# Optimization experiments

Hardware: AMD Instinct MI355X
Metric: run time of the kernel (lower is better)

Reference implementation:

```python
import jax, jax.numpy as jnp
import numpy as np

WIN = 9  # local window size per spatial dim

def _boxfilter3d(x):
    k = jnp.ones((1, 1, WIN, WIN, WIN), x.dtype) / float(WIN ** 3)
    return jax.lax.conv_general_dilated(
        x, k, window_strides=(1, 1, 1), padding='SAME',
        dimension_numbers=('NCDHW', 'OIDHW', 'NCDHW'))

def setup_inputs() -> dict:
    key = jax.random.key(0)
    k1, k2 = jax.random.split(key)
    shape = (2, 1, 160, 192, 160)
    y_true = jax.random.uniform(k1, shape, dtype=jnp.float32)
    y_pred = jax.random.uniform(k2, shape, dtype=jnp.float32)
    return {"y_true": y_true, "y_pred": y_pred}

def reference(y_true, y_pred):
    Ii, Ji = y_true, y_pred
    mu1 = _boxfilter3d(Ii)
    mu2 = _boxfilter3d(Ji)
    sigma1_sq = _boxfilter3d(Ii * Ii) - mu1 * mu1
    sigma2_sq = _boxfilter3d(Ji * Ji) - mu2 * mu2
    sigma12 = _boxfilter3d(Ii * Ji) - mu1 * mu2
    cc = (sigma12 * sigma12) / (sigma1_sq * sigma2_sq + 1e-5)
    return -jnp.mean(cc)
```

## Files before the change

### kernel.cpp

```cpp
#include <hip/hip_runtime.h>

#define DD 160
#define HH 192
#define WW 160
#define HWs (HH * WW)
#define NTOT 9830400.0f
#define DOUT 20
#define NIT  28
#define NBLK 960

#define SDRS 62
#define SDP  1492
#define HSRS 10
#define HSC  162
#define HSP  810

typedef float    v4 __attribute__((ext_vector_type(4)));
typedef _Float16 h4 __attribute__((ext_vector_type(4)));
typedef _Float16 h2 __attribute__((ext_vector_type(2)));
typedef _Float16 h8 __attribute__((ext_vector_type(8)));

__device__ __forceinline__ void block_sync_lds() {
    __builtin_amdgcn_s_waitcnt(0xc07f);
    __builtin_amdgcn_s_barrier();
}
__device__ __forceinline__ v4 up(h4 x) { return __builtin_convertvector(x, v4); }
__device__ __forceinline__ h4 dnp(v4 x) {
    h2 a = __builtin_bit_cast(h2, __builtin_amdgcn_cvt_pkrtz(x[0], x[1]));
    h2 b = __builtin_bit_cast(h2, __builtin_amdgcn_cvt_pkrtz(x[2], x[3]));
    return __builtin_shufflevector(a, b, 0, 1, 2, 3);
}

__global__ __launch_bounds__(256, 4) void kf(const float* __restrict__ I,
                                             const float* __restrict__ J,
                                             float* __restrict__ partial) {
    __shared__ __align__(16) h4 SDL[2 * SDP];
    __shared__ __align__(16) h4 HSL[2 * HSP];
    __shared__ float red[256];

    const int tid = threadIdx.x;
    const int bx = blockIdx.x, by = blockIdx.y, b = blockIdx.z;
    const int w0 = (bx % 5) * 32, h0 = (bx / 5) * 16;
    const int d0 = by * DOUT;
    const int bid = bx + 60 * (by + 8 * b);

    const int rt = tid ^ ((bx & 1) << 7);

    const bool p1 = rt < 240;
    const int r = rt / 10, g = rt % 10;
    const int gh = h0 - 4 + r, gw = w0 - 4 + g * 4;
    const bool colOK = p1 && gh >= 0 && gh < HH && gw >= 0 && gw < WW;
    const size_t colOff = (size_t)gh * WW + gw;
    const float* Ib = I + (size_t)b * DD * HWs + colOff;
    const float* Jb = J + (size_t)b * DD * HWs + colOff;
    const int sdwOff = r * SDRS + (r >> 3) * 2 + 6 * g;

    const bool p2 = rt < 100;
    const int g2 = rt % 10, ch2 = (rt / 10) % 5, hh0 = (rt / 50) * 8;
    const int sdrOff = hh0 * SDRS + (hh0 >> 3) * 2 + 6 * g2 +
                       (ch2 == 4 ? 4 + (g2 & 1) : ch2);
    const int hswOff = ch2 * HSC + hh0 * HSRS + g2;

    const bool p3 = rt >= 128;
    const int q3 = rt & 127;
    const int hh = q3 >> 3, sg = q3 & 7;
    const int hsrOff = hh * HSRS + sg;

    v4 sd0 = 0.f, sd1 = 0.f, sd2 = 0.f, sd3 = 0.f, sd4 = 0.f;
    h4 fI[10], fJ[10];
#pragma unroll
    for (int uu = 0; uu < 10; ++uu) { fI[uu] = (h4)(_Float16)0; fJ[uu] = (h4)(_Float16)0; }
    v4 pAI = 0.f, pAJ = 0.f, pBI = 0.f, pBJ = 0.f;
    float acc = 0.f;
    const float inv = 1.0f / 729.0f;

    {
        const int s0 = d0 - 4;
        if (colOK && s0 >= 0) {
            pAI = *(const v4*)(Ib + (size_t)s0 * HWs);
            pAJ = *(const v4*)(Jb + (size_t)s0 * HWs);
        }
        const int s1 = d0 - 3;
        if (colOK && s1 >= 0) {
            pBI = *(const v4*)(Ib + (size_t)s1 * HWs);
            pBJ = *(const v4*)(Jb + (size_t)s1 * HWs);
        }
    }

    for (int tb = 0; tb < 30; tb += 10) {
#pragma unroll
        for (int u = 0; u < 10; ++u) {
            const int t = tb + u;

            if (t < NIT && p1) {
                v4 curI, curJ;
                if ((u & 1) == 0) { curI = pAI; curJ = pAJ; }
                else              { curI = pBI; curJ = pBJ; }
                h4 cI = dnp(curI), cJ = dnp(curJ);
                v4 aI = up(cI), aJ = up(cJ);
                v4 dI = aI, dJv = aJ;
                v4 dII = aI * aI, dJJ = aJ * aJ, dIJ = aI * aJ;
                if (t >= 9) {
                    h4 oI = fI[(u + 1) % 10], oJ = fJ[(u + 1) % 10];
                    v4 bI = up(oI), bJ = up(oJ);
                    dI -= bI; dJv -= bJ;
                    dII -= bI * bI; dJJ -= bJ * bJ; dIJ -= bI * bJ;
                }
                fI[u] = cI; fJ[u] = cJ;
                sd0 += dI; sd1 += dJv; sd2 += dII; sd3 += dJJ; sd4 += dIJ;
                h4* const qb = &SDL[(t & 1) * SDP + sdwOff];
                h4 c0 = dnp(sd0), c1 = dnp(sd1), c2 = dnp(sd2), c3 = dnp(sd3);
                *(h8*)qb       = __builtin_shufflevector(c0, c1, 0,1,2,3,4,5,6,7);
                *(h8*)(qb + 2) = __builtin_shufflevector(c2, c3, 0,1,2,3,4,5,6,7);
                qb[4 + (g & 1)] = dnp(sd4);
                v4 nI = 0.f, nJ = 0.f;
                const int sn = d0 - 2 + t;
                if (t + 2 < NIT && colOK && sn >= 0 && sn < DD) {
                    nI = *(const v4*)(Ib + (size_t)sn * HWs);
                    nJ = *(const v4*)(Jb + (size_t)sn * HWs);
                }
                if ((u & 1) == 0) { pAI = nI; pAJ = nJ; }
                else              { pBI = nI; pBJ = nJ; }
            }

            if (t >= 1 && t <= NIT && p2) {
                const int par = (t - 1) & 1;
                const h4* const sdr = &SDL[par * SDP + sdrOff];
                h4* const hsw = &HSL[par * HSP + hswOff];
                h4 keep[7];
                h4 s = sdr[0];
                keep[0] = s;
#pragma unroll
                for (int k = 1; k < 9; ++k) {
                    h4 v = sdr[k * SDRS + (k >= 8 ? 2 : 0)];
                    if (k < 7) keep[k] = v;
                    s += v;
                }
                hsw[0] = s;
#pragma unroll
                for (int j = 1; j < 8; ++j) {
                    s += sdr[(j + 8) * SDRS + 2] - keep[j - 1];
                    hsw[j * HSRS] = s;
                }
            }

            if (t >= 10 && p3) {
                const h4* const hsr = &HSL[(t & 1) * HSP + hsrOff];
                float w[5][4];
#pragma unroll
                for (int c = 0; c < 5; ++c) {
                    v4 fa = up(hsr[c * HSC]);
                    v4 fb = up(hsr[c * HSC + 1]);
                    v4 fc = up(hsr[c * HSC + 2]);
                    float s = fa[0] + fa[1] + fa[2] + fa[3] +
                              fb[0] + fb[1] + fb[2] + fb[3] + fc[0];
                    w[c][0] = s;
                    s += fc[1] - fa[0]; w[c][1] = s;
                    s += fc[2] - fa[1]; w[c][2] = s;
                    s += fc[3] - fa[2]; w[c][3] = s;
                }
#pragma unroll
                for (int e = 0; e < 4; ++e) {
                    float mu1 = w[0][e] * inv, mu2 = w[1][e] * inv;
                    float g1  = fmaf(-mu1, mu1, w[2][e] * inv);
                    float g2v = fmaf(-mu2, mu2, w[3][e] * inv);
                    float g12 = fmaf(-mu1, mu2, w[4][e] * inv);
                    acc += __fdividef(g12 * g12, fmaf(g1, g2v, 1e-5f));
                }
            }

            block_sync_lds();
        }
    }

    red[tid] = acc;
    __syncthreads();
    if (tid < 128) red[tid] += red[tid + 128];
    __syncthreads();
    if (tid < 64) {
        float a = red[tid] + red[tid + 64];
#pragma unroll
        for (int off = 32; off > 0; off >>= 1) a += __shfl_down(a, off);
        if (tid == 0) partial[bid] = a;
    }
}

__global__ void k3_final(const float* __restrict__ partial,
                         float* __restrict__ out) {
    __shared__ float r[1024];
    const int i = threadIdx.x;
    r[i] = (i < NBLK) ? partial[i] : 0.f;
    __syncthreads();
    for (int off = 512; off > 0; off >>= 1) {
        if (i < off) r[i] += r[i + off];
        __syncthreads();
    }
    if (i == 0) out[0] = -r[0] * (1.0f / NTOT);
}

extern "C" void kernel_launch(void* const* d_in, const int* in_sizes, int n_in,
                              void* d_out, int out_size, void* d_ws, size_t ws_size,
                              hipStream_t stream) {
    (void)in_sizes; (void)n_in; (void)out_size; (void)ws_size;
    const float* I = (const float*)d_in[0];
    const float* J = (const float*)d_in[1];
    float* out     = (float*)d_out;
    float* partial = (float*)d_ws;

    dim3 grid(60, 8, 2);
    kf<<<grid, 256, 0, stream>>>(I, J, partial);
    k3_final<<<1, 1024, 0, stream>>>(partial, out);
}
```

Baseline: 163.0 us.

## Halve depth chunk per block, doubling grid, with single-slice prefetch and LDS re-reads

Reduces the output depth per block from 20 to 10 slices, so the grid doubles to 1920 blocks and each block iterates 18 steps instead of 28. The aim is more parallelism and better CU fill. The price is a larger share of halo work: each block now reads 18 input slices to produce 10 outputs, versus 28 for 20. The prefetch pipeline drops from two slices in flight to one, and the ring buffer shrinks to 9 entries. The H-sum stage now re-reads outgoing values from LDS instead of keeping them in registers, and the final reduction is extended to handle 1920 partials.

```diff
diff --git a/kernel.cpp b/kernel.cpp
--- a/kernel.cpp
+++ b/kernel.cpp
@@ -5,9 +5,9 @@
 #define WW 160
 #define HWs (HH * WW)
 #define NTOT 9830400.0f
-#define DOUT 20
-#define NIT  28
-#define NBLK 960
+#define DOUT 10
+#define NIT  18
+#define NBLK 1920
 
 #define SDRS 62
 #define SDP  1492
@@ -42,7 +42,7 @@
     const int bx = blockIdx.x, by = blockIdx.y, b = blockIdx.z;
     const int w0 = (bx % 5) * 32, h0 = (bx / 5) * 16;
     const int d0 = by * DOUT;
-    const int bid = bx + 60 * (by + 8 * b);
+    const int bid = bx + 60 * (by + 16 * b);
 
     const int rt = tid ^ ((bx & 1) << 7);
 
@@ -67,109 +67,95 @@
     const int hsrOff = hh * HSRS + sg;
 
     v4 sd0 = 0.f, sd1 = 0.f, sd2 = 0.f, sd3 = 0.f, sd4 = 0.f;
-    h4 fI[10], fJ[10];
-#pragma unroll
-    for (int uu = 0; uu < 10; ++uu) { fI[uu] = (h4)(_Float16)0; fJ[uu] = (h4)(_Float16)0; }
-    v4 pAI = 0.f, pAJ = 0.f, pBI = 0.f, pBJ = 0.f;
+    h4 fI[9], fJ[9];
+#pragma unroll
+    for (int uu = 0; uu < 9; ++uu) { fI[uu] = (h4)(_Float16)0; fJ[uu] = (h4)(_Float16)0; }
+    v4 pLI = 0.f, pLJ = 0.f;
     float acc = 0.f;
     const float inv = 1.0f / 729.0f;
 
     {
-        const int s0 = d0 - 4;
-        if (colOK && s0 >= 0) {
-            pAI = *(const v4*)(Ib + (size_t)s0 * HWs);
-            pAJ = *(const v4*)(Jb + (size_t)s0 * HWs);
+        const int si = d0 - 4;
+        if (colOK && si >= 0) {
+            pLI = *(const v4*)(Ib + (size_t)si * HWs);
+            pLJ = *(const v4*)(Jb + (size_t)si * HWs);
         }
-        const int s1 = d0 - 3;
-        if (colOK && s1 >= 0) {
-            pBI = *(const v4*)(Ib + (size_t)s1 * HWs);
-            pBJ = *(const v4*)(Jb + (size_t)s1 * HWs);
-        }
-    }
-
-    for (int tb = 0; tb < 30; tb += 10) {
-#pragma unroll
-        for (int u = 0; u < 10; ++u) {
+    }
+
+    for (int tb = 0; tb < 27; tb += 9) {
+#pragma unroll
+        for (int u = 0; u < 9; ++u) {
             const int t = tb + u;
-
-            if (t < NIT && p1) {
-                v4 curI, curJ;
-                if ((u & 1) == 0) { curI = pAI; curJ = pAJ; }
-                else              { curI = pBI; curJ = pBJ; }
-                h4 cI = dnp(curI), cJ = dnp(curJ);
-                v4 aI = up(cI), aJ = up(cJ);
-                v4 dI = aI, dJv = aJ;
-                v4 dII = aI * aI, dJJ = aJ * aJ, dIJ = aI * aJ;
-                if (t >= 9) {
-                    h4 oI = fI[(u + 1) % 10], oJ = fJ[(u + 1) % 10];
-                    v4 bI = up(oI), bJ = up(oJ);
-                    dI -= bI; dJv -= bJ;
-                    dII -= bI * bI; dJJ -= bJ * bJ; dIJ -= bI * bJ;
+            if (t < NIT + 2) {
+                if (t < NIT && p1) {
+                    h4 cI = dnp(pLI), cJ = dnp(pLJ);
+                    v4 aI = up(cI), aJ = up(cJ);
+                    v4 dI = aI, dJv = aJ;
+                    v4 dII = aI * aI, dJJ = aJ * aJ, dIJ = aI * aJ;
+                    if (t >= 9) {
+                        v4 bI = up(fI[u]), bJ = up(fJ[u]);
+                        dI -= bI; dJv -= bJ;
+                        dII -= bI * bI; dJJ -= bJ * bJ; dIJ -= bI * bJ;
+                    }
+                    fI[u] = cI; fJ[u] = cJ;
+                    sd0 += dI; sd1 += dJv; sd2 += dII; sd3 += dJJ; sd4 += dIJ;
+                    h4* const qb = &SDL[(t & 1) * SDP + sdwOff];
+                    h4 c0 = dnp(sd0), c1 = dnp(sd1), c2 = dnp(sd2), c3 = dnp(sd3);
+                    *(h8*)qb       = __builtin_shufflevector(c0, c1, 0,1,2,3,4,5,6,7);
+                    *(h8*)(qb + 2) = __builtin_shufflevector(c2, c3, 0,1,2,3,4,5,6,7);
+                    qb[4 + (g & 1)] = dnp(sd4);
+                    pLI = 0.f; pLJ = 0.f;
+                    const int sn = d0 - 3 + t;
+                    if (t + 1 < NIT && colOK && sn >= 0 && sn < DD) {
+                        pLI = *(const v4*)(Ib + (size_t)sn * HWs);
+                        pLJ = *(const v4*)(Jb + (size_t)sn * HWs);
+                    }
                 }
-                fI[u] = cI; fJ[u] = cJ;
-                sd0 += dI; sd1 += dJv; sd2 += dII; sd3 += dJJ; sd4 += dIJ;
-                h4* const qb = &SDL[(t & 1) * SDP + sdwOff];
-                h4 c0 = dnp(sd0), c1 = dnp(sd1), c2 = dnp(sd2), c3 = dnp(sd3);
-                *(h8*)qb       = __builtin_shufflevector(c0, c1, 0,1,2,3,4,5,6,7);
-                *(h8*)(qb + 2) = __builtin_shufflevector(c2, c3, 0,1,2,3,4,5,6,7);
-                qb[4 + (g & 1)] = dnp(sd4);
-                v4 nI = 0.f, nJ = 0.f;
-                const int sn = d0 - 2 + t;
-                if (t + 2 < NIT && colOK && sn >= 0 && sn < DD) {
-                    nI = *(const v4*)(Ib + (size_t)sn * HWs);
-                    nJ = *(const v4*)(Jb + (size_t)sn * HWs);
+
+                if (t >= 1 && t <= NIT && p2) {
+                    const int par = (t - 1) & 1;
+                    const h4* const sdr = &SDL[par * SDP + sdrOff];
+                    h4* const hsw = &HSL[par * HSP + hswOff];
+                    h4 s = sdr[0];
+#pragma unroll
+                    for (int k = 1; k < 9; ++k)
+                        s += sdr[k * SDRS + (k >= 8 ? 2 : 0)];
+                    hsw[0] = s;
+#pragma unroll
+                    for (int j = 1; j < 8; ++j) {
+                        s += sdr[(j + 8) * SDRS + 2]
+                           - sdr[(j - 1) * SDRS + (j - 1 >= 8 ? 2 : 0)];
+                        hsw[j * HSRS] = s;
+                    }
                 }
-                if ((u & 1) == 0) { pAI = nI; pAJ = nJ; }
-                else              { pBI = nI; pBJ = nJ; }
+
+                if (t >= 10 && p3) {
+                    const h4* const hsr = &HSL[(t & 1) * HSP + hsrOff];
+                    float w[5][4];
+#pragma unroll
+                    for (int c = 0; c < 5; ++c) {
+                        v4 fa = up(hsr[c * HSC]);
+                        v4 fb = up(hsr[c * HSC + 1]);
+                        v4 fc = up(hsr[c * HSC + 2]);
+                        float s = fa[0] + fa[1] + fa[2] + fa[3] +
+                                  fb[0] + fb[1] + fb[2] + fb[3] + fc[0];
+                        w[c][0] = s;
+                        s += fc[1] - fa[0]; w[c][1] = s;
+                        s += fc[2] - fa[1]; w[c][2] = s;
+                        s += fc[3] - fa[2]; w[c][3] = s;
+                    }
+#pragma unroll
+                    for (int e = 0; e < 4; ++e) {
+                        float mu1 = w[0][e] * inv, mu2 = w[1][e] * inv;
+                        float g1  = fmaf(-mu1, mu1, w[2][e] * inv);
+                        float g2v = fmaf(-mu2, mu2, w[3][e] * inv);
+                        float g12 = fmaf(-mu1, mu2, w[4][e] * inv);
+                        acc += __fdividef(g12 * g12, fmaf(g1, g2v, 1e-5f));
+                    }
+                }
+
+                block_sync_lds();
             }
-
-            if (t >= 1 && t <= NIT && p2) {
-                const int par = (t - 1) & 1;
-                const h4* const sdr = &SDL[par * SDP + sdrOff];
-                h4* const hsw = &HSL[par * HSP + hswOff];
-                h4 keep[7];
-                h4 s = sdr[0];
-                keep[0] = s;
-#pragma unroll
-                for (int k = 1; k < 9; ++k) {
-                    h4 v = sdr[k * SDRS + (k >= 8 ? 2 : 0)];
-                    if (k < 7) keep[k] = v;
-                    s += v;
-                }
-                hsw[0] = s;
-#pragma unroll
-                for (int j = 1; j < 8; ++j) {
-                    s += sdr[(j + 8) * SDRS + 2] - keep[j - 1];
-                    hsw[j * HSRS] = s;
-                }
-            }
-
-            if (t >= 10 && p3) {
-                const h4* const hsr = &HSL[(t & 1) * HSP + hsrOff];
-                float w[5][4];
-#pragma unroll
-                for (int c = 0; c < 5; ++c) {
-                    v4 fa = up(hsr[c * HSC]);
-                    v4 fb = up(hsr[c * HSC + 1]);
-                    v4 fc = up(hsr[c * HSC + 2]);
-                    float s = fa[0] + fa[1] + fa[2] + fa[3] +
-                              fb[0] + fb[1] + fb[2] + fb[3] + fc[0];
-                    w[c][0] = s;
-                    s += fc[1] - fa[0]; w[c][1] = s;
-                    s += fc[2] - fa[1]; w[c][2] = s;
-                    s += fc[3] - fa[2]; w[c][3] = s;
-                }
-#pragma unroll
-                for (int e = 0; e < 4; ++e) {
-                    float mu1 = w[0][e] * inv, mu2 = w[1][e] * inv;
-                    float g1  = fmaf(-mu1, mu1, w[2][e] * inv);
-                    float g2v = fmaf(-mu2, mu2, w[3][e] * inv);
-                    float g12 = fmaf(-mu1, mu2, w[4][e] * inv);
-                    acc += __fdividef(g12 * g12, fmaf(g1, g2v, 1e-5f));
-                }
-            }
-
-            block_sync_lds();
         }
     }
 
@@ -189,7 +175,9 @@
                          float* __restrict__ out) {
     __shared__ float r[1024];
     const int i = threadIdx.x;
-    r[i] = (i < NBLK) ? partial[i] : 0.f;
+    float v = (i < NBLK) ? partial[i] : 0.f;
+    if (i + 1024 < NBLK) v += partial[i + 1024];
+    r[i] = v;
     __syncthreads();
     for (int off = 512; off > 0; off >>= 1) {
         if (i < off) r[i] += r[i + off];
@@ -207,7 +195,7 @@
     float* out     = (float*)d_out;
     float* partial = (float*)d_ws;
 
-    dim3 grid(60, 8, 2);
+    dim3 grid(60, 16, 2);
     kf<<<grid, 256, 0, stream>>>(I, J, partial);
     k3_final<<<1, 1024, 0, stream>>>(partial, out);
 }
```

New measurement: 167.8 us. +3.0%, slower.
